# Kernel optimization log

Measured on AMD Instinct MI355X. Metric: run time of the kernel, lower is better.

Reference implementation:

```python
import jax, jax.numpy as jnp
import numpy as np

B, N, D, H, HD, FF, E, V, HID = 32, 125, 256, 8, 32, 1024, 5, 32000, 128
S = N + 3
MAXPOS = 512
EPS = 1e-12       # BERT LayerNorm eps
THRESH = 0.7


def setup_inputs() -> dict:
    key = jax.random.key(0)
    ks = iter(jax.random.split(key, 32))
    def rn(shape):
        return jax.random.normal(next(ks), shape, jnp.float32)
    def p(shape):
        return rn(shape) * 0.02
    inp = {
        "h_t": rn((B, D)),
        "e_task": rn((B, D)),
        "e_layout": rn((B, D)),
        "token_embeds": rn((B, N, D)),
        # router: Linear(768,128) -> ReLU -> Linear(128,5)
        "router_W1": p((3 * D, HID)), "router_b1": jnp.zeros((HID,), jnp.float32),
        "router_W2": p((HID, E)), "router_b2": jnp.zeros((E,), jnp.float32),
        "hint_W": p((D, E)), "hint_b": jnp.zeros((E,), jnp.float32),
        # per-expert BERT params, stacked over expert dim E
        "pos_emb": p((E, MAXPOS, D)),
        "type_emb": p((E, D)),                    # token_type_id=0 row only
        "ln_emb_g": jnp.ones((E, D), jnp.float32), "ln_emb_b": jnp.zeros((E, D), jnp.float32),
        "Wq": p((E, D, D)), "bq": jnp.zeros((E, D), jnp.float32),
        "Wk": p((E, D, D)), "bk": jnp.zeros((E, D), jnp.float32),
        "Wv": p((E, D, D)), "bv": jnp.zeros((E, D), jnp.float32),
        "Wo": p((E, D, D)), "bo": jnp.zeros((E, D), jnp.float32),
        "ln_attn_g": jnp.ones((E, D), jnp.float32), "ln_attn_b": jnp.zeros((E, D), jnp.float32),
        "Wf1": p((E, D, FF)), "bf1": jnp.zeros((E, FF), jnp.float32),
        "Wf2": p((E, FF, D)), "bf2": jnp.zeros((E, D), jnp.float32),
        "ln_ffn_g": jnp.ones((E, D), jnp.float32), "ln_ffn_b": jnp.zeros((E, D), jnp.float32),
        "head_W": p((D, V)), "head_b": jnp.zeros((V,), jnp.float32),
        "top_k": 2,
    }
    return inp


def _ln(x, g, b):
    m = jnp.mean(x, axis=-1, keepdims=True)
    v = jnp.mean(jnp.square(x - m), axis=-1, keepdims=True)
    return (x - m) * jax.lax.rsqrt(v + EPS) * g + b


def _expert(pos, typ, g0, b0, Wq, bq, Wk, bk, Wv, bv, Wo, bo, g1, b1,
            Wf1, bf1, Wf2, bf2, g2, b2, x):
    # 1-layer BERT encoder (eval mode, no causal mask for inputs_embeds).
    Bx, Sx, _ = x.shape
    h = _ln(x + pos[:Sx][None] + typ[None, None], g0, b0)        # [B,S,D]
    q = (h @ Wq + bq).reshape(Bx, Sx, H, HD)
    k = (h @ Wk + bk).reshape(Bx, Sx, H, HD)
    v = (h @ Wv + bv).reshape(Bx, Sx, H, HD)
    scores = jnp.einsum("bqhd,bkhd->bhqk", q, k) / np.float32(np.sqrt(HD))
    attn = jax.nn.softmax(scores, axis=-1)
    ctx = jnp.einsum("bhqk,bkhd->bqhd", attn, v).reshape(Bx, Sx, D)
    h = _ln(h + ctx @ Wo + bo, g1, b1)
    f = jax.nn.gelu(h @ Wf1 + bf1, approximate=False)
    h = _ln(h + f @ Wf2 + bf2, g2, b2)
    return h


def reference(h_t, e_task, e_layout, token_embeds,
              router_W1, router_b1, router_W2, router_b2, hint_W, hint_b,
              pos_emb, type_emb, ln_emb_g, ln_emb_b,
              Wq, bq, Wk, bk, Wv, bv, Wo, bo, ln_attn_g, ln_attn_b,
              Wf1, bf1, Wf2, bf2, ln_ffn_g, ln_ffn_b,
              head_W, head_b, top_k):
    prefix = jnp.stack([h_t, e_task, e_layout], axis=1)            # [B,3,D]
    x_t = jnp.concatenate([prefix, token_embeds], axis=1)          # [B,S,D]
    flat = jnp.concatenate([h_t, e_task, e_layout], axis=-1)       # [B,3D]
    gate_logits = (jax.nn.relu(flat @ router_W1 + router_b1) @ router_W2
                   + router_b2 + e_layout @ hint_W + hint_b)
    gate_probs = jax.nn.softmax(gate_logits, axis=-1)              # [B,E]
    topk_vals, topk_idx = jax.lax.top_k(gate_probs, top_k)         # [B,k]
    # k collapses to 1 only if EVERY row's max prob exceeds threshold
    use_k1 = jnp.all(jnp.max(gate_probs, axis=-1) > THRESH)
    keep = jnp.where(jnp.arange(top_k) == 0, 1.0,
                     jnp.where(use_k1, 0.0, 1.0)).astype(gate_probs.dtype)
    w = topk_vals * keep[None, :]                                  # [B,k]
    # run all experts densely (E=5 small), then gated combine
    expert_outs = jax.vmap(_expert, in_axes=(0,) * 20 + (None,))(
        pos_emb, type_emb, ln_emb_g, ln_emb_b,
        Wq, bq, Wk, bk, Wv, bv, Wo, bo, ln_attn_g, ln_attn_b,
        Wf1, bf1, Wf2, bf2, ln_ffn_g, ln_ffn_b, x_t)               # [E,B,S,D]
    onehot = jax.nn.one_hot(topk_idx, E, dtype=w.dtype)            # [B,k,E]
    comb = jnp.einsum("bk,bke->be", w, onehot)                     # [B,E]
    z = jnp.einsum("be,ebsd->bsd", comb, expert_outs)              # [B,S,D]
    logits = z @ head_W + head_b                                   # [B,S,V]
    return logits, gate_probs
```

## Files before the change

### kernel.cpp

```cpp
#include <hip/hip_runtime.h>
#include <hip/hip_bf16.h>
#include <math.h>

namespace {

constexpr int B = 32, N = 125, D = 256, H = 8, HD = 32, FF = 1024,
              E = 5, V = 32000, HID = 128, S = 128, MAXPOS = 512;
constexpr int BSD = B * S * D;
constexpr float EPS = 1e-12f;
constexpr float THRESH = 0.7f;

constexpr size_t GW_Q = 0, GW_K = 65536, GW_V = 131072, GW_O = 196608,
                 GW_F1 = 262144, GW_F2 = 524288, GW_STRIDE = 786432;

typedef __attribute__((ext_vector_type(4))) float f32x4;
typedef __attribute__((ext_vector_type(8))) short short8v;

__device__ __forceinline__ short f2bf(float f) {
  __hip_bfloat16 h = __float2bfloat16(f);
  short s;
  __builtin_memcpy(&s, &h, 2);
  return s;
}

__device__ __forceinline__ float gelu_exact(float x) {
  return 0.5f * x * (1.f + erff(x * 0.70710678118654752f));
}

__device__ __forceinline__ float wave_sum64(float v) {
#pragma unroll
  for (int off = 32; off > 0; off >>= 1) v += __shfl_xor(v, off);
  return v;
}

__device__ __forceinline__ void gload16(const void* g, void* l) {
  __builtin_amdgcn_global_load_lds(
      (const __attribute__((address_space(1))) unsigned int*)g,
      (__attribute__((address_space(3))) unsigned int*)l, 16, 0, 0);
}

__global__ __launch_bounds__(HID) void router1_kernel(
    const float* __restrict__ h_t, const float* __restrict__ e_task,
    const float* __restrict__ e_layout, const float* __restrict__ W1,
    const float* __restrict__ b1, const float* __restrict__ W2,
    const float* __restrict__ b2, const float* __restrict__ hintW,
    const float* __restrict__ hintb, float* __restrict__ gp_ws,
    float* __restrict__ gp_out) {
  int b = blockIdx.x;
  int t = threadIdx.x;
  float acc = b1[t];
  const float* rows[3] = {h_t + b * D, e_task + b * D, e_layout + b * D};
  for (int seg = 0; seg < 3; ++seg) {
    const float* r = rows[seg];
    const float* w = W1 + (size_t)seg * D * HID;
    for (int i = 0; i < D; ++i) acc += r[i] * w[i * HID + t];
  }
  __shared__ float hid[HID];
  __shared__ float logits[E];
  hid[t] = fmaxf(acc, 0.f);
  __syncthreads();
  if (t < E) {
    float l = b2[t] + hintb[t];
    for (int hh = 0; hh < HID; ++hh) l += hid[hh] * W2[hh * E + t];
    const float* el = e_layout + b * D;
    for (int dd = 0; dd < D; ++dd) l += el[dd] * hintW[dd * E + t];
    logits[t] = l;
  }
  __syncthreads();
  if (t == 0) {
    float mx = logits[0];
    for (int e2 = 1; e2 < E; ++e2) mx = fmaxf(mx, logits[e2]);
    float p[E];
    float se = 0.f;
    for (int e2 = 0; e2 < E; ++e2) {
      p[e2] = expf(logits[e2] - mx);
      se += p[e2];
    }
    float inv = 1.f / se;
    for (int e2 = 0; e2 < E; ++e2) {
      float pe = p[e2] * inv;
      gp_ws[b * E + e2] = pe;
      gp_out[b * E + e2] = pe;
    }
  }
}

__global__ __launch_bounds__(64) void router2_kernel(
    const float* __restrict__ gp, const int* __restrict__ topk_ptr,
    float* __restrict__ comb) {
  __shared__ int allk1;
  int t = threadIdx.x;
  if (t == 0) allk1 = 1;
  __syncthreads();
  float p[E];
  if (t < B) {
    float mx = 0.f;
    for (int e2 = 0; e2 < E; ++e2) {
      p[e2] = gp[t * E + e2];
      mx = fmaxf(mx, p[e2]);
    }
    if (!(mx > THRESH)) allk1 = 0;
  }
  __syncthreads();
  int k1 = allk1;
  if (t < B) {
    for (int e2 = 0; e2 < E; ++e2) comb[t * E + e2] = 0.f;
    int tk = *topk_ptr;
    if (tk > E) tk = E;
    float q[E];
    for (int e2 = 0; e2 < E; ++e2) q[e2] = p[e2];
    for (int kk = 0; kk < tk; ++kk) {
      int bi = 0;
      float bv = q[0];
      for (int e2 = 1; e2 < E; ++e2)
        if (q[e2] > bv) { bv = q[e2]; bi = e2; }
      float w = (kk == 0) ? bv : (k1 ? 0.f : bv);
      comb[t * E + bi] += w;
      q[bi] = -1.f;
    }
  }
}

__global__ __launch_bounds__(256) void prep_w(
    const float* __restrict__ W, short* __restrict__ G, int K, int Nc,
    size_t estrW, size_t estrG) {
  __shared__ float Wl[64][65];
  int t = threadIdx.x;
  int e = blockIdx.z;
  const float* Wp = W + (size_t)e * estrW;
  short* Gp = G + (size_t)e * estrG;
  int n0 = blockIdx.x * 64, k0 = blockIdx.y * 64;
#pragma unroll
  for (int p = 0; p < 4; ++p) {
    int krow = p * 16 + (t >> 4);
    int nc = (t & 15) * 4;
    float4 v = *reinterpret_cast<const float4*>(
        Wp + (size_t)(k0 + krow) * Nc + n0 + nc);
    Wl[krow][nc] = v.x; Wl[krow][nc + 1] = v.y;
    Wl[krow][nc + 2] = v.z; Wl[krow][nc + 3] = v.w;
  }
  __syncthreads();
#pragma unroll
  for (int p = 0; p < 2; ++p) {
    int gid = p * 256 + t;
    int nl = gid >> 3, kg = gid & 7;
    int xv = (nl >> 1) & 3;
    int bk = kg >> 2, s = kg & 3;
    int sp = s ^ xv;
    short8v o;
#pragma unroll
    for (int j = 0; j < 8; ++j) o[j] = f2bf(Wl[kg * 8 + j][nl]);
    *reinterpret_cast<short8v*>(
        Gp + (size_t)(n0 + nl) * K + ((k0 >> 5) + bk) * 32 + sp * 8) = o;
  }
}

__global__ __launch_bounds__(256) void embed_ln_w(
    const float* __restrict__ h_t, const float* __restrict__ e_task,
    const float* __restrict__ e_layout, const float* __restrict__ tok,
    const float* __restrict__ pos_b, const float* __restrict__ typ_b,
    const float* __restrict__ g_b, const float* __restrict__ bb_b,
    float* __restrict__ out_b, const float* __restrict__ comb) {
  int e = blockIdx.y;
  int t = threadIdx.x, lane = t & 63, w = t >> 6;
  int row = blockIdx.x * 4 + w;
  int b = row >> 7, s = row & 127;
  if (comb[b * E + e] == 0.f) return;
  const float* pos_e = pos_b + (size_t)e * MAXPOS * D;
  const float* typ_e = typ_b + (size_t)e * D;
  const float* g = g_b + (size_t)e * D;
  const float* bb = bb_b + (size_t)e * D;
  float* outp = out_b + (size_t)e * BSD;
  int d0 = lane * 4;
  const float* src = (s >= 3) ? tok + ((size_t)(b * N + s - 3)) * D
                   : (s == 0) ? h_t + (size_t)b * D
                   : (s == 1) ? e_task + (size_t)b * D
                              : e_layout + (size_t)b * D;
  float4 x = *reinterpret_cast<const float4*>(src + d0);
  float4 pe = *reinterpret_cast<const float4*>(pos_e + (size_t)s * D + d0);
  float4 te = *reinterpret_cast<const float4*>(typ_e + d0);
  x.x += pe.x + te.x; x.y += pe.y + te.y;
  x.z += pe.z + te.z; x.w += pe.w + te.w;
  float mean = wave_sum64(x.x + x.y + x.z + x.w) * (1.f / D);
  float4 xm = {x.x - mean, x.y - mean, x.z - mean, x.w - mean};
  float vv = wave_sum64(xm.x * xm.x + xm.y * xm.y + xm.z * xm.z + xm.w * xm.w);
  float rs = rsqrtf(vv * (1.f / D) + EPS);
  float4 g4 = *reinterpret_cast<const float4*>(g + d0);
  float4 b4 = *reinterpret_cast<const float4*>(bb + d0);
  float4 o = {xm.x * rs * g4.x + b4.x, xm.y * rs * g4.y + b4.y,
              xm.z * rs * g4.z + b4.z, xm.w * rs * g4.w + b4.w};
  *reinterpret_cast<float4*>(outp + (size_t)row * D + d0) = o;
}

__global__ __launch_bounds__(256) void add_ln_w(
    const float* __restrict__ A_b, const float* __restrict__ R_b,
    const float* __restrict__ g_b, const float* __restrict__ bb_b,
    float* __restrict__ out_b, const float* __restrict__ comb) {
  int e = blockIdx.y;
  int t = threadIdx.x, lane = t & 63, w = t >> 6;
  int row = blockIdx.x * 4 + w;
  int b = row >> 7;
  if (comb[b * E + e] == 0.f) return;
  const float* A = A_b + (size_t)e * BSD;
  const float* R = R_b + (size_t)e * BSD;
  const float* g = g_b + (size_t)e * D;
  const float* bb = bb_b + (size_t)e * D;
  float* outp = out_b + (size_t)e * BSD;
  int d0 = lane * 4;
  float4 a4 = *reinterpret_cast<const float4*>(A + (size_t)row * D + d0);
  float4 r4 = *reinterpret_cast<const float4*>(R + (size_t)row * D + d0);
  float4 x = {a4.x + r4.x, a4.y + r4.y, a4.z + r4.z, a4.w + r4.w};
  float mean = wave_sum64(x.x + x.y + x.z + x.w) * (1.f / D);
  float4 xm = {x.x - mean, x.y - mean, x.z - mean, x.w - mean};
  float vv = wave_sum64(xm.x * xm.x + xm.y * xm.y + xm.z * xm.z + xm.w * xm.w);
  float rs = rsqrtf(vv * (1.f / D) + EPS);
  float4 g4 = *reinterpret_cast<const float4*>(g + d0);
  float4 b4 = *reinterpret_cast<const float4*>(bb + d0);
  float4 o = {xm.x * rs * g4.x + b4.x, xm.y * rs * g4.y + b4.y,
              xm.z * rs * g4.z + b4.z, xm.w * rs * g4.w + b4.w};
  *reinterpret_cast<float4*>(outp + (size_t)row * D + d0) = o;
}

__global__ __launch_bounds__(128) void attn2_kernel(
    const float* __restrict__ Qb, const float* __restrict__ Kb,
    const float* __restrict__ Vb, float* __restrict__ Cb,
    const float* __restrict__ comb) {
  int e = blockIdx.y;
  int bh = blockIdx.x;
  int b = bh >> 3, h = bh & 7;
  if (comb[b * E + e] == 0.f) return;
  const float* Q = Qb + (size_t)e * BSD;
  const float* K = Kb + (size_t)e * BSD;
  const float* Vv = Vb + (size_t)e * BSD;
  float* C = Cb + (size_t)e * BSD;
  __shared__ float Ks[S][36];
  __shared__ float Vs[S][36];
  int t = threadIdx.x;
  const float* kb = K + ((size_t)(b * S + t)) * D + h * HD;
  const float* vb = Vv + ((size_t)(b * S + t)) * D + h * HD;
#pragma unroll
  for (int d = 0; d < HD; d += 4) {
    *reinterpret_cast<float4*>(&Ks[t][d]) =
        *reinterpret_cast<const float4*>(kb + d);
    *reinterpret_cast<float4*>(&Vs[t][d]) =
        *reinterpret_cast<const float4*>(vb + d);
  }
  float4 qv[8];
  const float* qp = Q + ((size_t)(b * S + t)) * D + h * HD;
#pragma unroll
  for (int j = 0; j < 8; ++j)
    qv[j] = *reinterpret_cast<const float4*>(qp + j * 4);
  __syncthreads();
  const float scale = 0.17677669529663687f;
  float mx = -1e30f;
  for (int k = 0; k < S; ++k) {
    float s = 0.f;
#pragma unroll
    for (int j = 0; j < 8; ++j) {
      float4 k4 = *reinterpret_cast<const float4*>(&Ks[k][j * 4]);
      s += qv[j].x * k4.x + qv[j].y * k4.y + qv[j].z * k4.z + qv[j].w * k4.w;
    }
    mx = fmaxf(mx, s * scale);
  }
  float se = 0.f;
  float4 cx[8];
#pragma unroll
  for (int j = 0; j < 8; ++j) cx[j] = {0.f, 0.f, 0.f, 0.f};
  for (int k = 0; k < S; ++k) {
    float s = 0.f;
#pragma unroll
    for (int j = 0; j < 8; ++j) {
      float4 k4 = *reinterpret_cast<const float4*>(&Ks[k][j * 4]);
      s += qv[j].x * k4.x + qv[j].y * k4.y + qv[j].z * k4.z + qv[j].w * k4.w;
    }
    float p = expf(s * scale - mx);
    se += p;
#pragma unroll
    for (int j = 0; j < 8; ++j) {
      float4 v4 = *reinterpret_cast<const float4*>(&Vs[k][j * 4]);
      cx[j].x += p * v4.x; cx[j].y += p * v4.y;
      cx[j].z += p * v4.z; cx[j].w += p * v4.w;
    }
  }
  float inv = 1.f / se;
  float* cp = C + ((size_t)(b * S + t)) * D + h * HD;
#pragma unroll
  for (int j = 0; j < 8; ++j) {
    float4 o = {cx[j].x * inv, cx[j].y * inv, cx[j].z * inv, cx[j].w * inv};
    *reinterpret_cast<float4*>(cp + j * 4) = o;
  }
}

template <int ACT, int K, int Nc, int ABF16, int OBF16>
__device__ __forceinline__ void gemm2_body(
    const char* __restrict__ Ag, const short* __restrict__ Gg,
    const float* __restrict__ bias, char* __restrict__ outp, int row0,
    int col0) {
  __shared__ short Al[128 * 40];
  __shared__ short Bl[128 * 32];
  const int t = threadIdx.x;
  const int lane = t & 63;
  const int w = t >> 6;
  const int wr = w >> 1, wc = w & 1;
  const int lrow = lane & 15;
  const int g = lane >> 4;
  const int lkoff = g * 8;
  const int koff = (g ^ ((lrow >> 1) & 3)) << 3;
  const char* Gb = (const char*)Gg;
  char* Bb = (char*)Bl;
  const int srow = t >> 2, sgrp = t & 3;
  const int woff = w * 1024;

  f32x4 acc[4][4];
#pragma unroll
  for (int m = 0; m < 4; ++m)
#pragma unroll
    for (int n = 0; n < 4; ++n) acc[m][n] = (f32x4){0.f, 0.f, 0.f, 0.f};

  for (int k0 = 0; k0 < K; k0 += 32) {
#pragma unroll
    for (int i = 0; i < 2; ++i) {
      int row = i * 64 + srow;
      gload16(Gb + (size_t)(col0 + row) * (K * 2) + (k0 >> 5) * 64 + sgrp * 16,
              Bb + i * 4096 + woff);
    }
    if (ABF16) {
      int row = t >> 1, c0 = (t & 1) * 2;
#pragma unroll
      for (int c = 0; c < 2; ++c) {
        short8v v = *reinterpret_cast<const short8v*>(
            (const short*)Ag + (size_t)(row0 + row) * K + k0 + (c0 + c) * 8);
        *reinterpret_cast<short8v*>(&Al[row * 40 + (c0 + c) * 8]) = v;
      }
    } else {
#pragma unroll
      for (int j = 0; j < 4; ++j) {
        int id = t + 256 * j;
        int row = id >> 3, s4 = id & 7;
        float4 a4 = *reinterpret_cast<const float4*>(
            (const float*)Ag + (size_t)(row0 + row) * K + k0 + s4 * 4);
        short4 p;
        p.x = f2bf(a4.x); p.y = f2bf(a4.y); p.z = f2bf(a4.z); p.w = f2bf(a4.w);
        *reinterpret_cast<short4*>(&Al[row * 40 + s4 * 4]) = p;
      }
    }
    __syncthreads();
    short8v af[4], bfv[4];
#pragma unroll
    for (int m = 0; m < 4; ++m)
      af[m] = *reinterpret_cast<const short8v*>(
          &Al[(wr * 64 + m * 16 + lrow) * 40 + lkoff]);
#pragma unroll
    for (int n = 0; n < 4; ++n)
      bfv[n] = *reinterpret_cast<const short8v*>(
          &Bl[(wc * 64 + n * 16 + lrow) * 32 + koff]);
#pragma unroll
    for (int m = 0; m < 4; ++m)
#pragma unroll
      for (int n = 0; n < 4; ++n)
        acc[m][n] = __builtin_amdgcn_mfma_f32_16x16x32_bf16(
            af[m], bfv[n], acc[m][n], 0, 0, 0);
    __syncthreads();
  }
#pragma unroll
  for (int n = 0; n < 4; ++n) {
    int col = col0 + wc * 64 + n * 16 + lrow;
    float bc = bias[col];
#pragma unroll
    for (int m = 0; m < 4; ++m) {
      int rbase = row0 + wr * 64 + m * 16 + g * 4;
      f32x4 v = acc[m][n];
#pragma unroll
      for (int r = 0; r < 4; ++r) {
        float o = v[r] + bc;
        if (ACT == 1) o = gelu_exact(o);
        if (OBF16)
          ((short*)outp)[(size_t)(rbase + r) * Nc + col] = f2bf(o);
        else
          ((float*)outp)[(size_t)(rbase + r) * Nc + col] = o;
      }
    }
  }
}

template <int ACT, int K, int Nc, int ABF16, int OBF16>
__global__ __launch_bounds__(256) void gemm2_e(
    const char* __restrict__ Ab, const short* __restrict__ Gbase,
    const float* __restrict__ biasb, char* __restrict__ outb,
    const float* __restrict__ comb, size_t aStrB, size_t oStrB, int bStr) {
  int e = blockIdx.z;
  int row0 = blockIdx.y * 128;
  int col0 = blockIdx.x * 128;
  if (comb[(row0 >> 7) * E + e] == 0.f) return;
  gemm2_body<ACT, K, Nc, ABF16, OBF16>(
      Ab + (size_t)e * aStrB, Gbase + (size_t)e * GW_STRIDE,
      biasb + (size_t)e * bStr, outb + (size_t)e * oStrB, row0, col0);
}

__global__ __launch_bounds__(256) void qkv2_e(
    const float* __restrict__ h0b, const short* __restrict__ Gw,
    const float* __restrict__ bqb, const float* __restrict__ bkb,
    const float* __restrict__ bvb, float* __restrict__ qb,
    float* __restrict__ kb, float* __restrict__ vb,
    const float* __restrict__ comb) {
  int e = blockIdx.z;
  int which = blockIdx.x >> 1;
  int col0 = (blockIdx.x & 1) * 128;
  int row0 = blockIdx.y * 128;
  if (comb[(row0 >> 7) * E + e] == 0.f) return;
  const short* G = Gw + (size_t)e * GW_STRIDE + (size_t)which * 65536;
  const float* bias =
      (which == 0 ? bqb : which == 1 ? bkb : bvb) + (size_t)e * D;
  float* outp = (which == 0 ? qb : which == 1 ? kb : vb) + (size_t)e * BSD;
  gemm2_body<0, D, D, 0, 0>((const char*)h0b + (size_t)e * BSD * 4, G, bias,
                            (char*)outp, row0, col0);
}

template <int ACT, int K, int Nc>
__device__ __forceinline__ void gemm_body(
    const float* __restrict__ Ag, const float* __restrict__ Wg,
    const float* __restrict__ bias, float* __restrict__ outp, int row0,
    int col0) {
  __shared__ short Al[128 * 40];
  __shared__ short Bl[128 * 40];
  const int t = threadIdx.x;
  const int lane = t & 63;
  const int w = t >> 6;
  const int wr = w >> 1, wc = w & 1;
  const int lrow = lane & 15;
  const int lkoff = (lane >> 4) * 8;
  f32x4 acc[4][4];
#pragma unroll
  for (int m = 0; m < 4; ++m)
#pragma unroll
    for (int n = 0; n < 4; ++n) acc[m][n] = (f32x4){0.f, 0.f, 0.f, 0.f};
  const int colB = t >> 1, kh = (t & 1) * 16;
  for (int k0 = 0; k0 < K; k0 += 32) {
#pragma unroll
    for (int j = 0; j < 4; ++j) {
      int id = t + 256 * j;
      int row = id >> 3, s4 = id & 7;
      float4 a4 = *reinterpret_cast<const float4*>(
          Ag + (size_t)(row0 + row) * K + k0 + s4 * 4);
      short4 p;
      p.x = f2bf(a4.x); p.y = f2bf(a4.y); p.z = f2bf(a4.z); p.w = f2bf(a4.w);
      *reinterpret_cast<short4*>(&Al[row * 40 + s4 * 4]) = p;
    }
    {
      const float* wp = Wg + (size_t)(k0 + kh) * Nc + (col0 + colB);
      short8v v0, v1;
#pragma unroll
      for (int kk = 0; kk < 8; ++kk) v0[kk] = f2bf(wp[(size_t)kk * Nc]);
#pragma unroll
      for (int kk = 0; kk < 8; ++kk) v1[kk] = f2bf(wp[(size_t)(kk + 8) * Nc]);
      *reinterpret_cast<short8v*>(&Bl[colB * 40 + kh]) = v0;
      *reinterpret_cast<short8v*>(&Bl[colB * 40 + kh + 8]) = v1;
    }
    __syncthreads();
    short8v af[4], bfv[4];
#pragma unroll
    for (int m = 0; m < 4; ++m)
      af[m] = *reinterpret_cast<const short8v*>(
          &Al[(wr * 64 + m * 16 + lrow) * 40 + lkoff]);
#pragma unroll
    for (int n = 0; n < 4; ++n)
      bfv[n] = *reinterpret_cast<const short8v*>(
          &Bl[(wc * 64 + n * 16 + lrow) * 40 + lkoff]);
#pragma unroll
    for (int m = 0; m < 4; ++m)
#pragma unroll
      for (int n = 0; n < 4; ++n)
        acc[m][n] = __builtin_amdgcn_mfma_f32_16x16x32_bf16(
            af[m], bfv[n], acc[m][n], 0, 0, 0);
    __syncthreads();
  }
#pragma unroll
  for (int n = 0; n < 4; ++n) {
    int col = col0 + wc * 64 + n * 16 + lrow;
    float bc = bias[col];
#pragma unroll
    for (int m = 0; m < 4; ++m) {
      int rbase = row0 + wr * 64 + m * 16 + (lane >> 4) * 4;
      f32x4 v = acc[m][n];
#pragma unroll
      for (int r = 0; r < 4; ++r) {
        float o = v[r] + bc;
        if (ACT == 1) o = gelu_exact(o);
        outp[(size_t)(rbase + r) * Nc + col] = o;
      }
    }
  }
}

__global__ __launch_bounds__(256) void head_gemm(
    const float* __restrict__ Ag, const float* __restrict__ Wg,
    const float* __restrict__ bias, float* __restrict__ outp) {
  int row0 = blockIdx.x * 128;
  int col0 = blockIdx.y * 128;
  gemm_body<0, D, V>(Ag, Wg, bias, outp, row0, col0);
}

template <int BF16>
__global__ __launch_bounds__(256) void combine_kernel(
    const float* __restrict__ hb, const float* __restrict__ comb,
    short* __restrict__ zs, float* __restrict__ zf) {
  size_t i = ((size_t)blockIdx.x * 256 + threadIdx.x) * 4;
  int b = (int)(i >> 15);
  float4 acc = {0.f, 0.f, 0.f, 0.f};
#pragma unroll
  for (int e2 = 0; e2 < E; ++e2) {
    float c = comb[b * E + e2];
    if (c != 0.f) {
      float4 v = *reinterpret_cast<const float4*>(hb + (size_t)e2 * BSD + i);
      acc.x += c * v.x; acc.y += c * v.y;
      acc.z += c * v.z; acc.w += c * v.w;
    }
  }
  if (BF16) {
    int row = (int)(i >> 8);
    int col = (int)(i & 255);
    int xv = (row >> 1) & 3;
    int colp = (col & ~24) | ((((col >> 3) & 3) ^ xv) << 3);
    short4 o;
    o.x = f2bf(acc.x); o.y = f2bf(acc.y); o.z = f2bf(acc.z); o.w = f2bf(acc.w);
    *reinterpret_cast<short4*>(zs + (size_t)row * 256 + colp) = o;
  } else {
    *reinterpret_cast<float4*>(zf + i) = acc;
  }
}

__global__ __launch_bounds__(256) void head_gemm2(
    const short* __restrict__ zs, const short* __restrict__ G,
    const float* __restrict__ bias, float* __restrict__ outp) {
  __shared__ short Al[128 * 32];
  __shared__ short Bl[128 * 32];
  const int row0 = blockIdx.x * 128;
  const int col0 = blockIdx.y * 128;
  const int t = threadIdx.x;
  const int lane = t & 63, w = t >> 6;
  const int wr = w >> 1, wc = w & 1;
  const int lrow = lane & 15;
  const int g = lane >> 4;
  const int koff = (g ^ ((lrow >> 1) & 3)) << 3;
  const int srow = t >> 2, sgrp = t & 3;
  const char* zsb = (const char*)zs;
  const char* Gb = (const char*)G;
  char* Ab = (char*)Al;
  char* Bb = (char*)Bl;
  const int woff = w * 1024;

  f32x4 acc[4][4];
#pragma unroll
  for (int m = 0; m < 4; ++m)
#pragma unroll
    for (int n = 0; n < 4; ++n) acc[m][n] = (f32x4){0.f, 0.f, 0.f, 0.f};

  for (int kb = 0; kb < 8; ++kb) {
#pragma unroll
    for (int i = 0; i < 2; ++i) {
      int row = i * 64 + srow;
      gload16(zsb + (size_t)(row0 + row) * 512 + kb * 64 + sgrp * 16,
              Ab + i * 4096 + woff);
      gload16(Gb + (size_t)(col0 + row) * 512 + kb * 64 + sgrp * 16,
              Bb + i * 4096 + woff);
    }
    __syncthreads();
    short8v af[4], bfv[4];
#pragma unroll
    for (int m = 0; m < 4; ++m)
      af[m] = *reinterpret_cast<const short8v*>(
          &Al[(wr * 64 + m * 16 + lrow) * 32 + koff]);
#pragma unroll
    for (int n = 0; n < 4; ++n)
      bfv[n] = *reinterpret_cast<const short8v*>(
          &Bl[(wc * 64 + n * 16 + lrow) * 32 + koff]);
#pragma unroll
    for (int m = 0; m < 4; ++m)
#pragma unroll
      for (int n = 0; n < 4; ++n)
        acc[m][n] = __builtin_amdgcn_mfma_f32_16x16x32_bf16(
            af[m], bfv[n], acc[m][n], 0, 0, 0);
    __syncthreads();
  }
#pragma unroll
  for (int n = 0; n < 4; ++n) {
    int col = col0 + wc * 64 + n * 16 + lrow;
    float bc = bias[col];
#pragma unroll
    for (int m = 0; m < 4; ++m) {
      int rbase = row0 + wr * 64 + m * 16 + g * 4;
      f32x4 v = acc[m][n];
#pragma unroll
      for (int r = 0; r < 4; ++r)
        outp[(size_t)(rbase + r) * V + col] = v[r] + bc;
    }
  }
}

}

extern "C" void kernel_launch(void* const* d_in, const int* in_sizes, int n_in,
                              void* d_out, int out_size, void* d_ws,
                              size_t ws_size, hipStream_t stream) {
  const float* h_t = (const float*)d_in[0];
  const float* e_task = (const float*)d_in[1];
  const float* e_layout = (const float*)d_in[2];
  const float* tok = (const float*)d_in[3];
  const float* rW1 = (const float*)d_in[4];
  const float* rb1 = (const float*)d_in[5];
  const float* rW2 = (const float*)d_in[6];
  const float* rb2 = (const float*)d_in[7];
  const float* hW = (const float*)d_in[8];
  const float* hb = (const float*)d_in[9];
  const float* pos = (const float*)d_in[10];
  const float* typ = (const float*)d_in[11];
  const float* g0 = (const float*)d_in[12];
  const float* b0 = (const float*)d_in[13];
  const float* Wq = (const float*)d_in[14];
  const float* bq = (const float*)d_in[15];
  const float* Wk = (const float*)d_in[16];
  const float* bk = (const float*)d_in[17];
  const float* Wv = (const float*)d_in[18];
  const float* bv = (const float*)d_in[19];
  const float* Wo = (const float*)d_in[20];
  const float* bo = (const float*)d_in[21];
  const float* g1 = (const float*)d_in[22];
  const float* b1 = (const float*)d_in[23];
  const float* Wf1 = (const float*)d_in[24];
  const float* bf1 = (const float*)d_in[25];
  const float* Wf2 = (const float*)d_in[26];
  const float* bf2 = (const float*)d_in[27];
  const float* g2 = (const float*)d_in[28];
  const float* b2 = (const float*)d_in[29];
  const float* headW = (const float*)d_in[30];
  const float* headb = (const float*)d_in[31];
  const int* topk = (const int*)d_in[32];

  float* out = (float*)d_out;
  float* gp_out = out + (size_t)B * S * V;

  float* h0 = out;
  float* qb2 = h0 + (size_t)E * BSD;
  float* kb2 = qb2 + (size_t)E * BSD;
  float* vb2 = kb2 + (size_t)E * BSD;
  float* ctxb = vb2 + (size_t)E * BSD;
  short* fbh = (short*)(ctxb + (size_t)E * BSD);
  short* Gw = (short*)(out + (size_t)25 * BSD + 10485760);

  float* wsf = (float*)d_ws;
  short* Ghead = (short*)d_ws;
  float* comb = wsf + 4096000;
  float* gp = comb + 256;
  short* zs = (short*)(wsf + 4096512);
  size_t need = (size_t)4096512 * 4 + (size_t)4096 * 256 * 2;
  bool fast_head = ws_size >= need;
  if (!fast_head) {
    comb = wsf;
    gp = comb + 256;
  }
  float* zf = gp + 256;

  if (fast_head)
    prep_w<<<dim3(V / 64, 4, 1), 256, 0, stream>>>(headW, Ghead, 256, V, 0, 0);
  prep_w<<<dim3(4, 4, E), 256, 0, stream>>>(Wq, Gw + GW_Q, 256, 256, 65536,
                                            GW_STRIDE);
  prep_w<<<dim3(4, 4, E), 256, 0, stream>>>(Wk, Gw + GW_K, 256, 256, 65536,
                                            GW_STRIDE);
  prep_w<<<dim3(4, 4, E), 256, 0, stream>>>(Wv, Gw + GW_V, 256, 256, 65536,
                                            GW_STRIDE);
  prep_w<<<dim3(4, 4, E), 256, 0, stream>>>(Wo, Gw + GW_O, 256, 256, 65536,
                                            GW_STRIDE);
  prep_w<<<dim3(16, 4, E), 256, 0, stream>>>(Wf1, Gw + GW_F1, 256, 1024,
                                             262144, GW_STRIDE);
  prep_w<<<dim3(4, 16, E), 256, 0, stream>>>(Wf2, Gw + GW_F2, 1024, 256,
                                             262144, GW_STRIDE);

  router1_kernel<<<B, HID, 0, stream>>>(h_t, e_task, e_layout, rW1, rb1, rW2,
                                        rb2, hW, hb, gp, gp_out);
  router2_kernel<<<1, 64, 0, stream>>>(gp, topk, comb);

  dim3 gLN(B * S / 4, E);
  embed_ln_w<<<gLN, 256, 0, stream>>>(h_t, e_task, e_layout, tok, pos, typ,
                                      g0, b0, h0, comb);
  qkv2_e<<<dim3(6, 32, E), 256, 0, stream>>>(h0, Gw, bq, bk, bv, qb2, kb2,
                                             vb2, comb);
  attn2_kernel<<<dim3(B * H, E), 128, 0, stream>>>(qb2, kb2, vb2, ctxb, comb);
  gemm2_e<0, 256, 256, 0, 0><<<dim3(2, 32, E), 256, 0, stream>>>(
      (const char*)ctxb, Gw + GW_O, bo, (char*)qb2, comb, (size_t)BSD * 4,
      (size_t)BSD * 4, 256);
  add_ln_w<<<gLN, 256, 0, stream>>>(h0, qb2, g1, b1, kb2, comb);
  gemm2_e<1, 256, 1024, 0, 1><<<dim3(8, 32, E), 256, 0, stream>>>(
      (const char*)kb2, Gw + GW_F1, bf1, (char*)fbh, comb, (size_t)BSD * 4,
      (size_t)B * S * FF * 2, FF);
  gemm2_e<0, 1024, 256, 1, 0><<<dim3(2, 32, E), 256, 0, stream>>>(
      (const char*)fbh, Gw + GW_F2, bf2, (char*)vb2, comb,
      (size_t)B * S * FF * 2, (size_t)BSD * 4, 256);
  add_ln_w<<<gLN, 256, 0, stream>>>(kb2, vb2, g2, b2, h0, comb);

  if (fast_head) {
    combine_kernel<1><<<BSD / 1024, 256, 0, stream>>>(h0, comb, zs, nullptr);
    head_gemm2<<<dim3(32, V / 128), 256, 0, stream>>>(zs, Ghead, headb, out);
  } else {
    combine_kernel<0><<<BSD / 1024, 256, 0, stream>>>(h0, comb, nullptr, zf);
    head_gemm<<<dim3(32, V / 128), 256, 0, stream>>>(zf, headW, headb, out);
  }
  (void)in_sizes; (void)n_in; (void)out_size;
}
```

Baseline: 452.8 us.

## Fuse final LayerNorm with expert combine, merge QKVO weight prep, use 64-row N=256 GEMMs

Fuses the second add+LayerNorm with the gated expert combine, so the per-expert normalized output is never written and re-read before the head GEMM. The four Q/K/V/O weight-prep launches become one kernel. The Wo and Wf2 GEMMs (N=256) switch to a 64-row tile variant that doubles the block count and improves occupancy on a narrow output. Trade-offs are a new GEMM body with its own tiling to maintain and smaller tiles that reuse weights less.

```diff
diff --git a/kernel.cpp b/kernel.cpp
--- a/kernel.cpp
+++ b/kernel.cpp
@@ -121,14 +121,11 @@
   }
 }
 
-__global__ __launch_bounds__(256) void prep_w(
-    const float* __restrict__ W, short* __restrict__ G, int K, int Nc,
-    size_t estrW, size_t estrG) {
+__device__ __forceinline__ void prep_body(const float* __restrict__ Wp,
+                                          short* __restrict__ Gp, int K,
+                                          int Nc) {
   __shared__ float Wl[64][65];
   int t = threadIdx.x;
-  int e = blockIdx.z;
-  const float* Wp = W + (size_t)e * estrW;
-  short* Gp = G + (size_t)e * estrG;
   int n0 = blockIdx.x * 64, k0 = blockIdx.y * 64;
 #pragma unroll
   for (int p = 0; p < 4; ++p) {
@@ -153,6 +150,26 @@
     *reinterpret_cast<short8v*>(
         Gp + (size_t)(n0 + nl) * K + ((k0 >> 5) + bk) * 32 + sp * 8) = o;
   }
+}
+
+__global__ __launch_bounds__(256) void prep_w(
+    const float* __restrict__ W, short* __restrict__ G, int K, int Nc,
+    size_t estrW, size_t estrG) {
+  int e = blockIdx.z;
+  prep_body(W + (size_t)e * estrW, G + (size_t)e * estrG, K, Nc);
+}
+
+__global__ __launch_bounds__(256) void prep_qkvo(
+    const float* __restrict__ Wq, const float* __restrict__ Wk,
+    const float* __restrict__ Wv, const float* __restrict__ Wo,
+    short* __restrict__ Gw) {
+  int z = blockIdx.z;
+  int e = z >> 2, which = z & 3;
+  const float* W =
+      (which == 0 ? Wq : which == 1 ? Wk : which == 2 ? Wv : Wo) +
+      (size_t)e * 65536;
+  short* G = Gw + (size_t)e * GW_STRIDE + (size_t)which * 65536;
+  prep_body(W, G, 256, 256);
 }
 
 __global__ __launch_bounds__(256) void embed_ln_w(
@@ -221,6 +238,49 @@
   *reinterpret_cast<float4*>(outp + (size_t)row * D + d0) = o;
 }
 
+template <int BF16>
+__global__ __launch_bounds__(256) void ln2_combine(
+    const float* __restrict__ A_b, const float* __restrict__ R_b,
+    const float* __restrict__ g_b, const float* __restrict__ bb_b,
+    const float* __restrict__ comb, short* __restrict__ zs,
+    float* __restrict__ zf) {
+  int t = threadIdx.x, lane = t & 63, w = t >> 6;
+  int row = blockIdx.x * 4 + w;
+  int b = row >> 7;
+  int d0 = lane * 4;
+  float4 z4 = {0.f, 0.f, 0.f, 0.f};
+  for (int e = 0; e < E; ++e) {
+    float c = comb[b * E + e];
+    if (c == 0.f) continue;
+    const float* A = A_b + (size_t)e * BSD + (size_t)row * D;
+    const float* R = R_b + (size_t)e * BSD + (size_t)row * D;
+    float4 a4 = *reinterpret_cast<const float4*>(A + d0);
+    float4 r4 = *reinterpret_cast<const float4*>(R + d0);
+    float4 x = {a4.x + r4.x, a4.y + r4.y, a4.z + r4.z, a4.w + r4.w};
+    float mean = wave_sum64(x.x + x.y + x.z + x.w) * (1.f / D);
+    float4 xm = {x.x - mean, x.y - mean, x.z - mean, x.w - mean};
+    float vv =
+        wave_sum64(xm.x * xm.x + xm.y * xm.y + xm.z * xm.z + xm.w * xm.w);
+    float rs = rsqrtf(vv * (1.f / D) + EPS);
+    float4 g4 = *reinterpret_cast<const float4*>(g_b + (size_t)e * D + d0);
+    float4 b4 = *reinterpret_cast<const float4*>(bb_b + (size_t)e * D + d0);
+    z4.x += c * (xm.x * rs * g4.x + b4.x);
+    z4.y += c * (xm.y * rs * g4.y + b4.y);
+    z4.z += c * (xm.z * rs * g4.z + b4.z);
+    z4.w += c * (xm.w * rs * g4.w + b4.w);
+  }
+  if (BF16) {
+    int col = d0;
+    int xv = (row >> 1) & 3;
+    int colp = (col & ~24) | ((((col >> 3) & 3) ^ xv) << 3);
+    short4 o;
+    o.x = f2bf(z4.x); o.y = f2bf(z4.y); o.z = f2bf(z4.z); o.w = f2bf(z4.w);
+    *reinterpret_cast<short4*>(zs + (size_t)row * 256 + colp) = o;
+  } else {
+    *reinterpret_cast<float4*>(zf + (size_t)row * D + d0) = z4;
+  }
+}
+
 __global__ __launch_bounds__(128) void attn2_kernel(
     const float* __restrict__ Qb, const float* __restrict__ Kb,
     const float* __restrict__ Vb, float* __restrict__ Cb,
@@ -384,6 +444,94 @@
 }
 
 template <int ACT, int K, int Nc, int ABF16, int OBF16>
+__device__ __forceinline__ void gemm2_body64(
+    const char* __restrict__ Ag, const short* __restrict__ Gg,
+    const float* __restrict__ bias, char* __restrict__ outp, int row0,
+    int col0) {
+  __shared__ short Al[64 * 40];
+  __shared__ short Bl[128 * 32];
+  const int t = threadIdx.x;
+  const int lane = t & 63;
+  const int w = t >> 6;
+  const int lrow = lane & 15;
+  const int g = lane >> 4;
+  const int lkoff = g * 8;
+  const int koff = (g ^ ((lrow >> 1) & 3)) << 3;
+  const char* Gb = (const char*)Gg;
+  char* Bb = (char*)Bl;
+  const int srow = t >> 2, sgrp = t & 3;
+  const int woff = w * 1024;
+
+  f32x4 acc[4][2];
+#pragma unroll
+  for (int m = 0; m < 4; ++m)
+#pragma unroll
+    for (int n = 0; n < 2; ++n) acc[m][n] = (f32x4){0.f, 0.f, 0.f, 0.f};
+
+  for (int k0 = 0; k0 < K; k0 += 32) {
+#pragma unroll
+    for (int i = 0; i < 2; ++i) {
+      int row = i * 64 + srow;
+      gload16(Gb + (size_t)(col0 + row) * (K * 2) + (k0 >> 5) * 64 + sgrp * 16,
+              Bb + i * 4096 + woff);
+    }
+    if (ABF16) {
+      int row = t >> 2, seg = t & 3;
+      short8v v = *reinterpret_cast<const short8v*>(
+          (const short*)Ag + (size_t)(row0 + row) * K + k0 + seg * 8);
+      *reinterpret_cast<short8v*>(&Al[row * 40 + seg * 8]) = v;
+    } else {
+#pragma unroll
+      for (int j = 0; j < 2; ++j) {
+        int id = t + 256 * j;
+        int row = id >> 3, s4 = id & 7;
+        float4 a4 = *reinterpret_cast<const float4*>(
+            (const float*)Ag + (size_t)(row0 + row) * K + k0 + s4 * 4);
+        short4 p;
+        p.x = f2bf(a4.x); p.y = f2bf(a4.y); p.z = f2bf(a4.z); p.w = f2bf(a4.w);
+        *reinterpret_cast<short4*>(&Al[row * 40 + s4 * 4]) = p;
+      }
+    }
+    __syncthreads();
+    short8v af[4], bfv[2];
+#pragma unroll
+    for (int m = 0; m < 4; ++m)
+      af[m] = *reinterpret_cast<const short8v*>(
+          &Al[(m * 16 + lrow) * 40 + lkoff]);
+#pragma unroll
+    for (int n = 0; n < 2; ++n)
+      bfv[n] = *reinterpret_cast<const short8v*>(
+          &Bl[(w * 32 + n * 16 + lrow) * 32 + koff]);
+#pragma unroll
+    for (int m = 0; m < 4; ++m)
+#pragma unroll
+      for (int n = 0; n < 2; ++n)
+        acc[m][n] = __builtin_amdgcn_mfma_f32_16x16x32_bf16(
+            af[m], bfv[n], acc[m][n], 0, 0, 0);
+    __syncthreads();
+  }
+#pragma unroll
+  for (int n = 0; n < 2; ++n) {
+    int col = col0 + w * 32 + n * 16 + lrow;
+    float bc = bias[col];
+#pragma unroll
+    for (int m = 0; m < 4; ++m) {
+      int rbase = row0 + m * 16 + g * 4;
+      f32x4 v = acc[m][n];
+#pragma unroll
+      for (int r = 0; r < 4; ++r) {
+        float o = v[r] + bc;
+        if (ACT == 1) o = gelu_exact(o);
+        if (OBF16)
+          ((short*)outp)[(size_t)(rbase + r) * Nc + col] = f2bf(o);
+        else
+          ((float*)outp)[(size_t)(rbase + r) * Nc + col] = o;
+      }
+    }
+  }
+}
+
+template <int ACT, int K, int Nc, int ABF16, int OBF16>
 __global__ __launch_bounds__(256) void gemm2_e(
     const char* __restrict__ Ab, const short* __restrict__ Gbase,
     const float* __restrict__ biasb, char* __restrict__ outb,
@@ -393,6 +541,20 @@
   int col0 = blockIdx.x * 128;
   if (comb[(row0 >> 7) * E + e] == 0.f) return;
   gemm2_body<ACT, K, Nc, ABF16, OBF16>(
+      Ab + (size_t)e * aStrB, Gbase + (size_t)e * GW_STRIDE,
+      biasb + (size_t)e * bStr, outb + (size_t)e * oStrB, row0, col0);
+}
+
+template <int ACT, int K, int Nc, int ABF16, int OBF16>
+__global__ __launch_bounds__(256) void gemm2b64_e(
+    const char* __restrict__ Ab, const short* __restrict__ Gbase,
+    const float* __restrict__ biasb, char* __restrict__ outb,
+    const float* __restrict__ comb, size_t aStrB, size_t oStrB, int bStr) {
+  int e = blockIdx.z;
+  int row0 = blockIdx.y * 64;
+  int col0 = blockIdx.x * 128;
+  if (comb[(row0 >> 7) * E + e] == 0.f) return;
+  gemm2_body64<ACT, K, Nc, ABF16, OBF16>(
       Ab + (size_t)e * aStrB, Gbase + (size_t)e * GW_STRIDE,
       biasb + (size_t)e * bStr, outb + (size_t)e * oStrB, row0, col0);
 }
@@ -498,35 +660,6 @@
   int row0 = blockIdx.x * 128;
   int col0 = blockIdx.y * 128;
   gemm_body<0, D, V>(Ag, Wg, bias, outp, row0, col0);
-}
-
-template <int BF16>
-__global__ __launch_bounds__(256) void combine_kernel(
-    const float* __restrict__ hb, const float* __restrict__ comb,
-    short* __restrict__ zs, float* __restrict__ zf) {
-  size_t i = ((size_t)blockIdx.x * 256 + threadIdx.x) * 4;
-  int b = (int)(i >> 15);
-  float4 acc = {0.f, 0.f, 0.f, 0.f};
-#pragma unroll
-  for (int e2 = 0; e2 < E; ++e2) {
-    float c = comb[b * E + e2];
-    if (c != 0.f) {
-      float4 v = *reinterpret_cast<const float4*>(hb + (size_t)e2 * BSD + i);
-      acc.x += c * v.x; acc.y += c * v.y;
-      acc.z += c * v.z; acc.w += c * v.w;
-    }
-  }
-  if (BF16) {
-    int row = (int)(i >> 8);
-    int col = (int)(i & 255);
-    int xv = (row >> 1) & 3;
-    int colp = (col & ~24) | ((((col >> 3) & 3) ^ xv) << 3);
-    short4 o;
-    o.x = f2bf(acc.x); o.y = f2bf(acc.y); o.z = f2bf(acc.z); o.w = f2bf(acc.w);
-    *reinterpret_cast<short4*>(zs + (size_t)row * 256 + colp) = o;
-  } else {
-    *reinterpret_cast<float4*>(zf + i) = acc;
-  }
 }
 
 __global__ __launch_bounds__(256) void head_gemm2(
@@ -595,6 +728,24 @@
         outp[(size_t)(rbase + r) * V + col] = v[r] + bc;
     }
   }
+}
+
+__global__ __launch_bounds__(256) void combine_f32(
+    const float* __restrict__ hb, const float* __restrict__ comb,
+    float* __restrict__ zf) {
+  size_t i = ((size_t)blockIdx.x * 256 + threadIdx.x) * 4;
+  int b = (int)(i >> 15);
+  float4 acc = {0.f, 0.f, 0.f, 0.f};
+#pragma unroll
+  for (int e2 = 0; e2 < E; ++e2) {
+    float c = comb[b * E + e2];
+    if (c != 0.f) {
+      float4 v = *reinterpret_cast<const float4*>(hb + (size_t)e2 * BSD + i);
+      acc.x += c * v.x; acc.y += c * v.y;
+      acc.z += c * v.z; acc.w += c * v.w;
+    }
+  }
+  *reinterpret_cast<float4*>(zf + i) = acc;
 }
 
 }
@@ -662,14 +813,7 @@
 
   if (fast_head)
     prep_w<<<dim3(V / 64, 4, 1), 256, 0, stream>>>(headW, Ghead, 256, V, 0, 0);
-  prep_w<<<dim3(4, 4, E), 256, 0, stream>>>(Wq, Gw + GW_Q, 256, 256, 65536,
-                                            GW_STRIDE);
-  prep_w<<<dim3(4, 4, E), 256, 0, stream>>>(Wk, Gw + GW_K, 256, 256, 65536,
-                                            GW_STRIDE);
-  prep_w<<<dim3(4, 4, E), 256, 0, stream>>>(Wv, Gw + GW_V, 256, 256, 65536,
-                                            GW_STRIDE);
-  prep_w<<<dim3(4, 4, E), 256, 0, stream>>>(Wo, Gw + GW_O, 256, 256, 65536,
-                                            GW_STRIDE);
+  prep_qkvo<<<dim3(4, 4, E * 4), 256, 0, stream>>>(Wq, Wk, Wv, Wo, Gw);
   prep_w<<<dim3(16, 4, E), 256, 0, stream>>>(Wf1, Gw + GW_F1, 256, 1024,
                                              262144, GW_STRIDE);
   prep_w<<<dim3(4, 16, E), 256, 0, stream>>>(Wf2, Gw + GW_F2, 1024, 256,
@@ -685,23 +829,24 @@
   qkv2_e<<<dim3(6, 32, E), 256, 0, stream>>>(h0, Gw, bq, bk, bv, qb2, kb2,
                                              vb2, comb);
   attn2_kernel<<<dim3(B * H, E), 128, 0, stream>>>(qb2, kb2, vb2, ctxb, comb);
-  gemm2_e<0, 256, 256, 0, 0><<<dim3(2, 32, E), 256, 0, stream>>>(
+  gemm2b64_e<0, 256, 256, 0, 0><<<dim3(2, 64, E), 256, 0, stream>>>(
       (const char*)ctxb, Gw + GW_O, bo, (char*)qb2, comb, (size_t)BSD * 4,
       (size_t)BSD * 4, 256);
   add_ln_w<<<gLN, 256, 0, stream>>>(h0, qb2, g1, b1, kb2, comb);
   gemm2_e<1, 256, 1024, 0, 1><<<dim3(8, 32, E), 256, 0, stream>>>(
       (const char*)kb2, Gw + GW_F1, bf1, (char*)fbh, comb, (size_t)BSD * 4,
       (size_t)B * S * FF * 2, FF);
-  gemm2_e<0, 1024, 256, 1, 0><<<dim3(2, 32, E), 256, 0, stream>>>(
+  gemm2b64_e<0, 1024, 256, 1, 0><<<dim3(2, 64, E), 256, 0, stream>>>(
       (const char*)fbh, Gw + GW_F2, bf2, (char*)vb2, comb,
       (size_t)B * S * FF * 2, (size_t)BSD * 4, 256);
-  add_ln_w<<<gLN, 256, 0, stream>>>(kb2, vb2, g2, b2, h0, comb);
 
   if (fast_head) {
-    combine_kernel<1><<<BSD / 1024, 256, 0, stream>>>(h0, comb, zs, nullptr);
+    ln2_combine<1><<<B * S / 4, 256, 0, stream>>>(kb2, vb2, g2, b2, comb, zs,
+                                                  nullptr);
     head_gemm2<<<dim3(32, V / 128), 256, 0, stream>>>(zs, Ghead, headb, out);
   } else {
-    combine_kernel<0><<<BSD / 1024, 256, 0, stream>>>(h0, comb, nullptr, zf);
+    add_ln_w<<<gLN, 256, 0, stream>>>(kb2, vb2, g2, b2, h0, comb);
+    combine_f32<<<BSD / 1024, 256, 0, stream>>>(h0, comb, zf);
     head_gemm<<<dim3(32, V / 128), 256, 0, stream>>>(zf, headW, headb, out);
   }
   (void)in_sizes; (void)n_in; (void)out_size;
```

Measured after the change: 434.5 us. 4.0% less time.
